# Kernel optimization log

Hardware: AMD Instinct MI355X
Metric: run time of the kernel (lower is better)

## Reference

```python
import jax, jax.numpy as jnp
import numpy as np

GRID_SIZE = 3
SPLINE_ORDER = 3
N_BASIS = GRID_SIZE + SPLINE_ORDER  # 6


def make_grid(in_features, dtype=jnp.float32):
    # efficient-kan grid buffer: extended uniform knots over grid_range=[-1, 1]
    h = 2.0 / GRID_SIZE
    g = jnp.arange(-SPLINE_ORDER, GRID_SIZE + SPLINE_ORDER + 1, dtype=dtype) * h - 1.0
    return jnp.tile(g[None, :], (in_features, 1))  # (in, G + 2S + 1)


def b_splines(x, grid):
    # x: (N, in), grid: (in, G+2S+1) -> (N, in, G+S) via Cox-de Boor recursion
    xb = x[..., None]
    bases = ((xb >= grid[:, :-1]) & (xb < grid[:, 1:])).astype(x.dtype)
    for k in range(1, SPLINE_ORDER + 1):
        bases = ((xb - grid[:, : -(k + 1)]) / (grid[:, k:-1] - grid[:, : -(k + 1)]) * bases[..., :-1]
                 + (grid[:, k + 1:] - xb) / (grid[:, k + 1:] - grid[:, 1:-k]) * bases[..., 1:])
    return bases


def kan_linear(x, base_w, spline_w, scaler, grid):
    # base path: silu(x) @ W_base^T ; spline path: contraction of basis with scaled spline weights
    base = jax.nn.silu(x) @ base_w.T
    scaled_sw = spline_w * scaler[..., None]  # (out, in, K)
    spl = jnp.einsum('nik,oik->no', b_splines(x, grid), scaled_sw)
    return base + spl


def setup_inputs() -> dict:
    key = jax.random.key(0)
    ks = jax.random.split(key, 7)
    B, C, P, D, H = 8, 8, 128, 256, 1024
    s = 0.05
    return {
        'x': jax.random.normal(ks[0], (B, C, P, D), dtype=jnp.float32),
        'base_w1': s * jax.random.normal(ks[1], (H, D), dtype=jnp.float32),
        'spline_w1': s * jax.random.normal(ks[2], (H, D, N_BASIS), dtype=jnp.float32),
        'scaler1': 1.0 + s * jax.random.normal(ks[3], (H, D), dtype=jnp.float32),
        'base_w2': s * jax.random.normal(ks[4], (D, H), dtype=jnp.float32),
        'spline_w2': s * jax.random.normal(ks[5], (D, H, N_BASIS), dtype=jnp.float32),
        'scaler2': 1.0 + s * jax.random.normal(ks[6], (D, H), dtype=jnp.float32),
    }


def reference(x, base_w1, spline_w1, scaler1, base_w2, spline_w2, scaler2):
    B, C, P, D = x.shape
    H = base_w1.shape[0]
    xf = x.reshape(-1, D)  # KANLinear flattens leading dims to tokens
    g1 = make_grid(D, x.dtype)
    g2 = make_grid(H, x.dtype)
    h = kan_linear(xf, base_w1, spline_w1, scaler1, g1)
    h = jax.nn.gelu(h, approximate=False)  # torch F.gelu default = exact erf
    # dropout is identity in eval / with p used as inference baseline
    y = kan_linear(h, base_w2, spline_w2, scaler2, g2)
    return y.reshape(B, C, P, D)
```

## Files before the change

### kernel.cpp

```cpp
#include <hip/hip_runtime.h>
#include <hip/hip_bf16.h>
#include <math.h>


typedef __attribute__((ext_vector_type(8))) short bf16x8;
typedef __attribute__((ext_vector_type(4))) float f32x4;

#define TOKENS 8192
#define D_IN   256
#define D_HID  1024

__device__ __forceinline__ void kan_features(float x, float f[8]) {
    f[0] = x * __builtin_amdgcn_rcpf(1.0f + __expf(-x));
    const float s = (x + 1.0f) * 1.5f + 3.0f;
    const float cf = floorf(s);
    const float u = s - cf;
    const int c = (int)cf;
    const float u2 = u * u, u3 = u2 * u;
    const float k6 = 1.0f / 6.0f;
    const float v3 = u3 * k6;
    const float v2 = (-3.0f * u3 + 3.0f * u2 + 3.0f * u + 1.0f) * k6;
    const float v1 = (3.0f * u3 - 6.0f * u2 + 4.0f) * k6;
    const float w1 = 1.0f - u;
    const float v0 = w1 * w1 * w1 * k6;
    const bool in = (s >= 0.0f) && (s < 9.0f);
#pragma unroll
    for (int j = 0; j < 6; ++j) {
        int d = c - j;
        float bv = (d == 0) ? v3 : (d == 1) ? v2 : (d == 2) ? v1 : (d == 3) ? v0 : 0.0f;
        f[1 + j] = in ? bv : 0.0f;
    }
    f[7] = 0.0f;
}

__device__ __forceinline__ void features_to_bf16(const float f[8], __hip_bfloat16 fb[8]) {
#pragma unroll
    for (int j = 0; j < 8; ++j) fb[j] = __float2bfloat16(f[j]);
}

__global__ void init_fused(const float* __restrict__ X, __hip_bfloat16* __restrict__ F,
                           const float* __restrict__ bw1, const float* __restrict__ sw1,
                           const float* __restrict__ sc1, __hip_bfloat16* __restrict__ W1,
                           const float* __restrict__ bw2, const float* __restrict__ sw2,
                           const float* __restrict__ sc2, __hip_bfloat16* __restrict__ W2) {
    const int b = blockIdx.x;
    if (b < 8192) {
        int idx = b * 256 + threadIdx.x;
        float f[8];
        kan_features(X[idx], f);
        __hip_bfloat16 fb[8];
        features_to_bf16(f, fb);
        *(bf16x8*)&F[(size_t)idx * 8] = *(bf16x8*)fb;
        return;
    }
    const bool w1 = (b < 9216);
    int idx = (w1 ? (b - 8192) : (b - 9216)) * 256 + threadIdx.x;
    const float* bw = w1 ? bw1 : bw2;
    const float* sw = w1 ? sw1 : sw2;
    const float* sc = w1 ? sc1 : sc2;
    __hip_bfloat16* Wo = w1 ? W1 : W2;
    float scl = sc[idx];
    __hip_bfloat16 row[8];
    row[0] = __float2bfloat16(bw[idx]);
#pragma unroll
    for (int j = 0; j < 6; ++j)
        row[1 + j] = __float2bfloat16(sw[idx * 6 + j] * scl);
    row[7] = __float2bfloat16(0.0f);
    *(bf16x8*)&Wo[(size_t)idx * 8] = *(bf16x8*)row;
}

#define GLL(src, dst) __builtin_amdgcn_global_load_lds(                         \
    (const __attribute__((address_space(1))) void*)(src),                       \
    (__attribute__((address_space(3))) void*)(dst), 16, 0, 0)

__global__ __launch_bounds__(256, 2)
void kan_gemm1(const __hip_bfloat16* __restrict__ A,
               const __hip_bfloat16* __restrict__ W,
               __hip_bfloat16* __restrict__ H) {
    constexpr int K = D_IN * 8;
    constexpr int NT = K / 64;
    __shared__ __hip_bfloat16 Al[2][128 * 64];
    __shared__ __hip_bfloat16 Bl[2][128 * 64];

    const int tid = threadIdx.x;
    const int wid = tid >> 6, lane = tid & 63;
    const int wm = wid >> 1, wn = wid & 1;
    const int lr = lane & 15, lg = lane >> 4;
    const int n0 = blockIdx.x * 128, o0 = blockIdx.y * 128;

    int srow[4], sslot[4];
#pragma unroll
    for (int p = 0; p < 4; ++p) {
        int item = tid + p * 256;
        srow[p] = item >> 3;
        sslot[p] = (item & 7) ^ (srow[p] & 7);
    }
    int aoff[2][4], boff[2][4];
#pragma unroll
    for (int ks = 0; ks < 2; ++ks)
#pragma unroll
        for (int f = 0; f < 4; ++f) {
            int ar = wm * 64 + f * 16 + lr;
            int br = wn * 64 + f * 16 + lr;
            aoff[ks][f] = ar * 64 + (((ks * 4 + lg) ^ (ar & 7)) * 8);
            boff[ks][f] = br * 64 + (((ks * 4 + lg) ^ (br & 7)) * 8);
        }

    f32x4 acc[4][4] = {};

#define STG1(buf, kt)                                                           \
    do {                                                                        \
        _Pragma("unroll")                                                       \
        for (int p = 0; p < 4; ++p) {                                           \
            GLL(A + (size_t)(n0 + srow[p]) * K + (kt) * 64 + sslot[p] * 8,      \
                &Al[buf][(tid + p * 256) * 8]);                                 \
            GLL(W + (size_t)(o0 + srow[p]) * K + (kt) * 64 + sslot[p] * 8,      \
                &Bl[buf][(tid + p * 256) * 8]);                                 \
        }                                                                       \
    } while (0)

    STG1(0, 0);
    STG1(1, 1);
    for (int t = 0; t < NT; ++t) {
        const int cur = t & 1;
        asm volatile("s_waitcnt vmcnt(8)" ::: "memory");
        __builtin_amdgcn_s_barrier();
        __builtin_amdgcn_sched_barrier(0);
        __builtin_amdgcn_s_setprio(1);
#pragma unroll
        for (int ks = 0; ks < 2; ++ks) {
            bf16x8 af[4], bfr[4];
#pragma unroll
            for (int f = 0; f < 4; ++f) af[f] = *(const bf16x8*)&Al[cur][aoff[ks][f]];
#pragma unroll
            for (int f = 0; f < 4; ++f) bfr[f] = *(const bf16x8*)&Bl[cur][boff[ks][f]];
#pragma unroll
            for (int fm = 0; fm < 4; ++fm)
#pragma unroll
                for (int fn = 0; fn < 4; ++fn)
                    acc[fm][fn] = __builtin_amdgcn_mfma_f32_16x16x32_bf16(
                        af[fm], bfr[fn], acc[fm][fn], 0, 0, 0);
        }
        __builtin_amdgcn_s_setprio(0);
        asm volatile("s_waitcnt lgkmcnt(0)" ::: "memory");
        __builtin_amdgcn_s_barrier();
        __builtin_amdgcn_sched_barrier(0);
        const int kn = (t + 2 < NT) ? t + 2 : NT - 1;
        STG1(cur, kn);
    }
#undef STG1
#pragma unroll
    for (int fm = 0; fm < 4; ++fm) {
#pragma unroll
        for (int fn = 0; fn < 4; ++fn) {
            int col = o0 + wn * 64 + fn * 16 + lr;
#pragma unroll
            for (int r = 0; r < 4; ++r) {
                int row = n0 + wm * 64 + fm * 16 + lg * 4 + r;
                float v = acc[fm][fn][r];
                float g = 0.5f * v * (1.0f + erff(v * 0.70710678118f));
                H[(size_t)row * D_HID + col] = __float2bfloat16(g);
            }
        }
    }
}

__global__ __launch_bounds__(512, 2)
void kan_gemm2(const __hip_bfloat16* __restrict__ H,
               const __hip_bfloat16* __restrict__ W,
               float* __restrict__ P) {
    constexpr int OUT = D_IN, KD = D_HID * 8;
    constexpr int NTT = KD / 64;
    __shared__ __hip_bfloat16 Al[128 * 64];
    __shared__ __hip_bfloat16 Bl[256 * 64];

    const int tid = threadIdx.x;
    const int wid = tid >> 6, lane = tid & 63;
    const int wm = wid >> 2, wn = wid & 3;
    const int lr = lane & 15, lg = lane >> 4;
    const int n0 = blockIdx.x * 128;

    const int per = NTT / 8;
    const int ks0 = blockIdx.z * per, ks1 = ks0 + per;

    int srow[4], sslot[4];
#pragma unroll
    for (int p = 0; p < 4; ++p) {
        int item = tid + p * 512;
        srow[p] = item >> 3;
        sslot[p] = (item & 7) ^ (srow[p] & 7);
    }
    const int ar0 = tid >> 3, ac = tid & 7;
    const __hip_bfloat16* hp0 = H + (size_t)(n0 + ar0) * D_HID + ac;
    const __hip_bfloat16* hp1 = H + (size_t)(n0 + ar0 + 64) * D_HID + ac;
    const int aw0 = ar0 * 64 + ((ac ^ (ar0 & 7)) * 8);
    const int aw1 = (ar0 + 64) * 64 + ((ac ^ (ar0 & 7)) * 8);

    int aoff[2][4], boff[2][4];
#pragma unroll
    for (int ks = 0; ks < 2; ++ks)
#pragma unroll
        for (int f = 0; f < 4; ++f) {
            int ar = wm * 64 + f * 16 + lr;
            int br = wn * 64 + f * 16 + lr;
            aoff[ks][f] = ar * 64 + (((ks * 4 + lg) ^ (ar & 7)) * 8);
            boff[ks][f] = br * 64 + (((ks * 4 + lg) ^ (br & 7)) * 8);
        }

    f32x4 acc[4][4] = {};

    float hv0 = __bfloat162float(hp0[(size_t)ks0 * 8]);
    float hv1 = __bfloat162float(hp1[(size_t)ks0 * 8]);

    for (int kt = ks0; kt < ks1; ++kt) {
        float hc0 = hv0, hc1 = hv1;
        const int knext = (kt + 1 < ks1) ? kt + 1 : ks1 - 1;
        hv0 = __bfloat162float(hp0[(size_t)knext * 8]);
        hv1 = __bfloat162float(hp1[(size_t)knext * 8]);
        {
            float ff[8]; __hip_bfloat16 fb[8];
            kan_features(hc0, ff); features_to_bf16(ff, fb);
            *(bf16x8*)&Al[aw0] = *(bf16x8*)fb;
            kan_features(hc1, ff); features_to_bf16(ff, fb);
            *(bf16x8*)&Al[aw1] = *(bf16x8*)fb;
        }
#pragma unroll
        for (int p = 0; p < 4; ++p)
            GLL(W + (size_t)srow[p] * KD + (size_t)kt * 64 + sslot[p] * 8,
                &Bl[(tid + p * 512) * 8]);
        __syncthreads();
#pragma unroll
        for (int ks = 0; ks < 2; ++ks) {
            bf16x8 af[4], bfr[4];
#pragma unroll
            for (int f = 0; f < 4; ++f) af[f] = *(const bf16x8*)&Al[aoff[ks][f]];
#pragma unroll
            for (int f = 0; f < 4; ++f) bfr[f] = *(const bf16x8*)&Bl[boff[ks][f]];
#pragma unroll
            for (int fm = 0; fm < 4; ++fm)
#pragma unroll
                for (int fn = 0; fn < 4; ++fn)
                    acc[fm][fn] = __builtin_amdgcn_mfma_f32_16x16x32_bf16(
                        af[fm], bfr[fn], acc[fm][fn], 0, 0, 0);
        }
        __syncthreads();
    }

    float* Pl = (float*)Bl;
    const size_t zoff = (size_t)blockIdx.z * TOKENS * OUT;
#pragma unroll
    for (int q = 0; q < 4; ++q) {
        __syncthreads();
        if (wm == (q >> 1)) {
#pragma unroll
            for (int fp = 0; fp < 2; ++fp) {
                int fm = (q & 1) * 2 + fp;
#pragma unroll
                for (int fn = 0; fn < 4; ++fn) {
                    int c = wn * 64 + fn * 16 + lr;
#pragma unroll
                    for (int r = 0; r < 4; ++r)
                        Pl[(fp * 16 + lg * 4 + r) * 256 + c] = acc[fm][fn][r];
                }
            }
        }
        __syncthreads();
#pragma unroll
        for (int p = 0; p < 4; ++p) {
            int v = tid + p * 512;
            int row = v >> 6, cv = (v & 63) * 4;
            *(f32x4*)&P[zoff + (size_t)(n0 + q * 32 + row) * OUT + cv] =
                *(const f32x4*)&Pl[row * 256 + cv];
        }
    }
}

__global__ void reduce_split(const float* __restrict__ P, float* __restrict__ out,
                             int nvec) {
    int i = blockIdx.x * 256 + threadIdx.x;
    if (i >= nvec) return;
    const f32x4* Pv = (const f32x4*)P;
    f32x4 s = Pv[i];
#pragma unroll
    for (int z = 1; z < 8; ++z) s += Pv[(size_t)z * nvec + i];
    ((f32x4*)out)[i] = s;
}

extern "C" void kernel_launch(void* const* d_in, const int* in_sizes, int n_in,
                              void* d_out, int out_size, void* d_ws, size_t ws_size,
                              hipStream_t stream) {
    const float* x   = (const float*)d_in[0];
    const float* bw1 = (const float*)d_in[1];
    const float* sw1 = (const float*)d_in[2];
    const float* sc1 = (const float*)d_in[3];
    const float* bw2 = (const float*)d_in[4];
    const float* sw2 = (const float*)d_in[5];
    const float* sc2 = (const float*)d_in[6];
    float* out = (float*)d_out;

    char* ws = (char*)d_ws;
    __hip_bfloat16* W1 = (__hip_bfloat16*)ws;
    __hip_bfloat16* W2 = (__hip_bfloat16*)(ws + (4ull << 20));
    __hip_bfloat16* F1 = (__hip_bfloat16*)(ws + (8ull << 20));
    __hip_bfloat16* Hb = (__hip_bfloat16*)(ws + (40ull << 20));
    float*          Pp = (float*)(ws + (72ull << 20));

    if (ws_size < (136ull << 20)) return;

    init_fused<<<10240, 256, 0, stream>>>(x, F1, bw1, sw1, sc1, W1, bw2, sw2, sc2, W2);

    kan_gemm1<<<dim3(TOKENS / 128, D_HID / 128), 256, 0, stream>>>(F1, W1, Hb);

    kan_gemm2<<<dim3(TOKENS / 128, 1, 8), 512, 0, stream>>>(Hb, W2, Pp);

    const int nvec = TOKENS * D_IN / 4;
    reduce_split<<<(nvec + 255) / 256, 256, 0, stream>>>(Pp, out, nvec);
}
```

Baseline: 136.7 us.

## Double-buffer W tiles in gemm2 with prefetch two stages ahead

Changes the second KAN GEMM to double-buffer the weight tile in LDS and issue global-to-LDS loads two K-steps ahead. Partial vmcnt waits replace the full syncthreads so loads overlap the MFMA work, and s_setprio raises priority during the MFMA section. The extra 32KB of LDS per block may reduce occupancy below the launch-bound target, and the hand-written waitcnt counts are fragile.

New measurement: 167.6 us. 22.6% more time.

```diff
diff --git a/kernel.cpp b/kernel.cpp
--- a/kernel.cpp
+++ b/kernel.cpp
@@ -172,7 +172,7 @@
     constexpr int OUT = D_IN, KD = D_HID * 8;
     constexpr int NTT = KD / 64;
     __shared__ __hip_bfloat16 Al[128 * 64];
-    __shared__ __hip_bfloat16 Bl[256 * 64];
+    __shared__ __hip_bfloat16 Bl[2][256 * 64];
 
     const int tid = threadIdx.x;
     const int wid = tid >> 6, lane = tid & 63;
@@ -209,33 +209,46 @@
 
     f32x4 acc[4][4] = {};
 
-    float hv0 = __bfloat162float(hp0[(size_t)ks0 * 8]);
-    float hv1 = __bfloat162float(hp1[(size_t)ks0 * 8]);
-
-    for (int kt = ks0; kt < ks1; ++kt) {
-        float hc0 = hv0, hc1 = hv1;
-        const int knext = (kt + 1 < ks1) ? kt + 1 : ks1 - 1;
-        hv0 = __bfloat162float(hp0[(size_t)knext * 8]);
-        hv1 = __bfloat162float(hp1[(size_t)knext * 8]);
-        {
-            float ff[8]; __hip_bfloat16 fb[8];
-            kan_features(hc0, ff); features_to_bf16(ff, fb);
-            *(bf16x8*)&Al[aw0] = *(bf16x8*)fb;
-            kan_features(hc1, ff); features_to_bf16(ff, fb);
-            *(bf16x8*)&Al[aw1] = *(bf16x8*)fb;
-        }
-#pragma unroll
-        for (int p = 0; p < 4; ++p)
-            GLL(W + (size_t)srow[p] * KD + (size_t)kt * 64 + sslot[p] * 8,
-                &Bl[(tid + p * 512) * 8]);
-        __syncthreads();
+#define STGB(buf, kt)                                                           \
+    do {                                                                        \
+        _Pragma("unroll")                                                       \
+        for (int p = 0; p < 4; ++p)                                             \
+            GLL(W + (size_t)srow[p] * KD + (size_t)(kt) * 64 + sslot[p] * 8,    \
+                &Bl[buf][(tid + p * 512) * 8]);                                 \
+    } while (0)
+
+#define FEAT(h0, h1)                                                            \
+    do {                                                                        \
+        float ff[8]; __hip_bfloat16 fb[8];                                      \
+        kan_features(h0, ff); features_to_bf16(ff, fb);                         \
+        *(bf16x8*)&Al[aw0] = *(bf16x8*)fb;                                      \
+        kan_features(h1, ff); features_to_bf16(ff, fb);                         \
+        *(bf16x8*)&Al[aw1] = *(bf16x8*)fb;                                      \
+    } while (0)
+
+    {
+        float h0 = __bfloat162float(hp0[(size_t)ks0 * 8]);
+        float h1 = __bfloat162float(hp1[(size_t)ks0 * 8]);
+        FEAT(h0, h1);
+    }
+    STGB(0, ks0);
+    __hip_bfloat16 hv0 = hp0[(size_t)(ks0 + 1) * 8];
+    __hip_bfloat16 hv1 = hp1[(size_t)(ks0 + 1) * 8];
+    STGB(1, ks0 + 1);
+
+    for (int t = ks0; t < ks1; ++t) {
+        const int cur = t & 1;
+        asm volatile("s_waitcnt vmcnt(6) lgkmcnt(0)" ::: "memory");
+        __builtin_amdgcn_s_barrier();
+        __builtin_amdgcn_sched_barrier(0);
+        __builtin_amdgcn_s_setprio(1);
 #pragma unroll
         for (int ks = 0; ks < 2; ++ks) {
             bf16x8 af[4], bfr[4];
 #pragma unroll
             for (int f = 0; f < 4; ++f) af[f] = *(const bf16x8*)&Al[aoff[ks][f]];
 #pragma unroll
-            for (int f = 0; f < 4; ++f) bfr[f] = *(const bf16x8*)&Bl[boff[ks][f]];
+            for (int f = 0; f < 4; ++f) bfr[f] = *(const bf16x8*)&Bl[cur][boff[ks][f]];
 #pragma unroll
             for (int fm = 0; fm < 4; ++fm)
 #pragma unroll
@@ -243,10 +256,26 @@
                     acc[fm][fn] = __builtin_amdgcn_mfma_f32_16x16x32_bf16(
                         af[fm], bfr[fn], acc[fm][fn], 0, 0, 0);
         }
-        __syncthreads();
-    }
-
-    float* Pl = (float*)Bl;
+        __builtin_amdgcn_s_setprio(0);
+        __builtin_amdgcn_s_barrier();
+        __builtin_amdgcn_sched_barrier(0);
+        {
+            float h0 = __bfloat162float(hv0);
+            float h1 = __bfloat162float(hv1);
+            FEAT(h0, h1);
+        }
+        const int hn = (t + 2 < ks1) ? t + 2 : ks1 - 1;
+        hv0 = hp0[(size_t)hn * 8];
+        hv1 = hp1[(size_t)hn * 8];
+        STGB(cur, hn);
+    }
+#undef STGB
+#undef FEAT
+
+    asm volatile("s_waitcnt vmcnt(0)" ::: "memory");
+    __builtin_amdgcn_s_barrier();
+
+    float* Pl = (float*)&Bl[0][0];
     const size_t zoff = (size_t)blockIdx.z * TOKENS * OUT;
 #pragma unroll
     for (int q = 0; q < 4; ++q) {
```
